# Performance work log

Measured on AMD Instinct MI355X. Metric: run time of the kernel, lower is better.

Reference implementation:

```python
import jax, jax.numpy as jnp
import numpy as np

H = W = 256  # hard-coded in the original nn.Fold(output_size=(256,256))


def _shift(x, dy, dx):
    """out[y, x] = x[y - dy, x - dx], zero outside. x: [B, H, W]."""
    xp = jnp.pad(x, ((0, 0), (1, 1), (1, 1)))
    return jax.lax.dynamic_slice(xp, (0, 1 - dy, 1 - dx), x.shape)


def setup_inputs() -> dict:
    key = jax.random.key(0)
    k1, k2, k3 = jax.random.split(key, 3)
    B = 64
    return {
        "affinity": jax.random.normal(k1, (B, 8, H, W), dtype=jnp.float32),
        "current_segmentation": jax.random.normal(k2, (B, 1, H, W), dtype=jnp.float32),
        "coarse_segmentation": jax.random.normal(k3, (B, 1, H, W), dtype=jnp.float32),
    }


def reference(affinity, current_segmentation, coarse_segmentation):
    # Normalize affinities by L1 sum over the 8 neighbor channels.
    abs_sum = jnp.sum(jnp.abs(affinity), axis=1, keepdims=True)
    raw_sum = jnp.sum(affinity, axis=1, keepdims=True)  # computed pre-normalization, as in source
    a = affinity / abs_sum
    # 9-tap spatially-varying kernel: 8 neighbors + synthesized center weight (1 - raw_sum).
    new_aff = jnp.concatenate([a[:, 0:4], 1.0 - raw_sum, a[:, 4:]], axis=1)  # [B,9,H,W]

    cur = current_segmentation[:, 0]  # [B,H,W]
    coa = coarse_segmentation[:, 0]   # [B,H,W]

    # unfold(seg)[k] at patch center q is seg[q + off_k]; fold scatters term_k[q] to q + off_k.
    out = jnp.zeros_like(cur)
    for k in range(9):
        dy, dx = k // 3 - 1, k % 3 - 1
        seg_k = coa if k == 4 else _shift(cur, -dy, -dx)   # gather neighbor (center from coarse)
        out = out + _shift(new_aff[:, k] * seg_k, dy, dx)  # overlap-add (fold)
    return out[:, None, :, :]  # [B,1,256,256]
```

## Files before the change

kernel.cpp:

```cpp
#include <hip/hip_runtime.h>

#define HH 256
#define WW 256
#define CC 8
#define TY 32
#define LW (WW + 2)
#define NSTRIP (HH / TY)

__global__ __launch_bounds__(256) void cspn_strip(
    const float* __restrict__ aff,
    const float* __restrict__ cur,
    const float* __restrict__ coa,
    float* __restrict__ out)
{
    __shared__ float ring[4][CC][LW];

    const int cpx = gridDim.x >> 3;
    int wg = blockIdx.x;
    wg = (wg & 7) * cpx + (wg >> 3);

    const int b  = wg >> 3;
    const int y0 = (wg & (NSTRIP - 1)) * TY;
    const int x  = threadIdx.x;

    if (threadIdx.x < 64) {
        const int s = threadIdx.x >> 4;
        const int c = (threadIdx.x >> 1) & 7;
        ring[s][c][(threadIdx.x & 1) ? (LW - 1) : 0] = 0.f;
    }

    const size_t plane = (size_t)HH * WW;
    const float* __restrict__ ab = aff + (size_t)b * CC * plane;
    const size_t img = (size_t)b * plane;

    float r[CC];
    {
        const int yy = y0 - 1;
        const bool inb = ((unsigned)yy < HH);
        #pragma unroll
        for (int c = 0; c < CC; ++c)
            r[c] = inb ? ab[c * plane + (size_t)yy * WW + x] : 0.f;
    }
    float rsum_prev = 0.f;

    __syncthreads();

    for (int y = y0 - 1; y <= y0 + TY; ++y) {
        float n[CC];
        const int yn = y + 1;
        const bool ldn = (yn <= y0 + TY) && ((unsigned)yn < HH);
        #pragma unroll
        for (int c = 0; c < CC; ++c)
            n[c] = ldn ? ab[c * plane + (size_t)yn * WW + x] : 0.f;

        const int j = y - 1;
        const bool emit = (j >= y0);
        float cj = 0.f, oj = 0.f;
        if (emit) {
            cj = cur[img + (size_t)j * WW + x];
            oj = coa[img + (size_t)j * WW + x];
        }

        float s = 0.f, rs = 0.f;
        #pragma unroll
        for (int c = 0; c < CC; ++c) { s += fabsf(r[c]); rs += r[c]; }
        const float invs = (s > 0.f) ? (1.0f / s) : 0.f;
        const int slot = (y + 4) & 3;
        #pragma unroll
        for (int c = 0; c < CC; ++c) ring[slot][c][x + 1] = r[c] * invs;

        __syncthreads();

        if (emit) {
            const int sp = (y + 4) & 3;
            const int sc = (y + 3) & 3;
            const int sm = (y + 2) & 3;
            const int xc = x + 1;
            const float sum =
                ring[sp][0][xc + 1] + ring[sp][1][xc] + ring[sp][2][xc - 1] +
                ring[sc][3][xc + 1]                   + ring[sc][4][xc - 1] +
                ring[sm][5][xc + 1] + ring[sm][6][xc] + ring[sm][7][xc - 1];
            out[img + (size_t)j * WW + x] = cj * sum + oj * (1.0f - rsum_prev);
        }

        rsum_prev = rs;
        #pragma unroll
        for (int c = 0; c < CC; ++c) r[c] = n[c];
    }
}

extern "C" void kernel_launch(void* const* d_in, const int* in_sizes, int n_in,
                              void* d_out, int out_size, void* d_ws, size_t ws_size,
                              hipStream_t stream) {
    const float* aff = (const float*)d_in[0];
    const float* cur = (const float*)d_in[1];
    const float* coa = (const float*)d_in[2];
    float* out = (float*)d_out;

    dim3 grid(64 * NSTRIP);
    dim3 block(256);
    cspn_strip<<<grid, block, 0, stream>>>(aff, cur, coa, out);
}
```

Measured before the change: 37.05 us.

## Process two rows per iteration with 512-thread blocks and six-slot ring

Each block now runs 512 threads, and the two 256-thread halves handle adjacent rows of the strip. This halves the serial loop trip count and the number of barriers per row. The ring buffer grows to six slots, and the raw per-pixel sum moves into shared memory so the previous row's sum can be read across thread groups. It costs more shared memory per block and adds modulo-6 slot arithmetic, and the larger blocks may lower the number of resident blocks.

```diff
diff --git a/kernel.cpp b/kernel.cpp
--- a/kernel.cpp
+++ b/kernel.cpp
@@ -7,13 +7,14 @@
 #define LW (WW + 2)
 #define NSTRIP (HH / TY)
 
-__global__ __launch_bounds__(256) void cspn_strip(
+__global__ __launch_bounds__(512, 4) void cspn_pair(
     const float* __restrict__ aff,
     const float* __restrict__ cur,
     const float* __restrict__ coa,
     float* __restrict__ out)
 {
-    __shared__ float ring[4][CC][LW];
+    __shared__ float ring[6][CC][LW];
+    __shared__ float rsring[6][WW];
 
     const int cpx = gridDim.x >> 3;
     int wg = blockIdx.x;
@@ -21,39 +22,41 @@
 
     const int b  = wg >> 3;
     const int y0 = (wg & (NSTRIP - 1)) * TY;
-    const int x  = threadIdx.x;
+    const int x  = threadIdx.x & 255;
+    const int g  = threadIdx.x >> 8;
 
-    if (threadIdx.x < 64) {
+    if (threadIdx.x < 96) {
         const int s = threadIdx.x >> 4;
-        const int c = (threadIdx.x >> 1) & 7;
-        ring[s][c][(threadIdx.x & 1) ? (LW - 1) : 0] = 0.f;
+        const int r = threadIdx.x & 15;
+        ring[s][r >> 1][(r & 1) ? (LW - 1) : 0] = 0.f;
     }
 
     const size_t plane = (size_t)HH * WW;
     const float* __restrict__ ab = aff + (size_t)b * CC * plane;
     const size_t img = (size_t)b * plane;
 
-    float r[CC];
+    float r_[CC];
     {
-        const int yy = y0 - 1;
+        const int yy = y0 - 1 + g;
         const bool inb = ((unsigned)yy < HH);
         #pragma unroll
         for (int c = 0; c < CC; ++c)
-            r[c] = inb ? ab[c * plane + (size_t)yy * WW + x] : 0.f;
+            r_[c] = inb ? ab[c * plane + (size_t)yy * WW + x] : 0.f;
     }
-    float rsum_prev = 0.f;
-
     __syncthreads();
 
-    for (int y = y0 - 1; y <= y0 + TY; ++y) {
-        float n[CC];
-        const int yn = y + 1;
+    for (int i = 0; i <= TY / 2; ++i) {
+        const int ya   = y0 - 1 + 2 * i;
+        const int yrow = ya + g;
+
+        float n_[CC];
+        const int yn = yrow + 2;
         const bool ldn = (yn <= y0 + TY) && ((unsigned)yn < HH);
         #pragma unroll
         for (int c = 0; c < CC; ++c)
-            n[c] = ldn ? ab[c * plane + (size_t)yn * WW + x] : 0.f;
+            n_[c] = ldn ? ab[c * plane + (size_t)yn * WW + x] : 0.f;
 
-        const int j = y - 1;
+        const int j = ya - 1 + g;
         const bool emit = (j >= y0);
         float cj = 0.f, oj = 0.f;
         if (emit) {
@@ -63,29 +66,30 @@
 
         float s = 0.f, rs = 0.f;
         #pragma unroll
-        for (int c = 0; c < CC; ++c) { s += fabsf(r[c]); rs += r[c]; }
+        for (int c = 0; c < CC; ++c) { s += fabsf(r_[c]); rs += r_[c]; }
         const float invs = (s > 0.f) ? (1.0f / s) : 0.f;
-        const int slot = (y + 4) & 3;
+        const int slot = (yrow + 12) % 6;
         #pragma unroll
-        for (int c = 0; c < CC; ++c) ring[slot][c][x + 1] = r[c] * invs;
+        for (int c = 0; c < CC; ++c) ring[slot][c][x + 1] = r_[c] * invs;
+        rsring[slot][x] = rs;
 
         __syncthreads();
 
         if (emit) {
-            const int sp = (y + 4) & 3;
-            const int sc = (y + 3) & 3;
-            const int sm = (y + 2) & 3;
+            const int sp = slot;
+            int sc = slot - 1; if (sc < 0) sc += 6;
+            int sm = slot - 2; if (sm < 0) sm += 6;
             const int xc = x + 1;
             const float sum =
                 ring[sp][0][xc + 1] + ring[sp][1][xc] + ring[sp][2][xc - 1] +
                 ring[sc][3][xc + 1]                   + ring[sc][4][xc - 1] +
                 ring[sm][5][xc + 1] + ring[sm][6][xc] + ring[sm][7][xc - 1];
-            out[img + (size_t)j * WW + x] = cj * sum + oj * (1.0f - rsum_prev);
+            const float rsj = rsring[sc][x];
+            out[img + (size_t)j * WW + x] = cj * sum + oj * (1.0f - rsj);
         }
 
-        rsum_prev = rs;
         #pragma unroll
-        for (int c = 0; c < CC; ++c) r[c] = n[c];
+        for (int c = 0; c < CC; ++c) r_[c] = n_[c];
     }
 }
 
@@ -98,6 +102,6 @@
     float* out = (float*)d_out;
 
     dim3 grid(64 * NSTRIP);
-    dim3 block(256);
-    cspn_strip<<<grid, block, 0, stream>>>(aff, cur, coa, out);
+    dim3 block(512);
+    cspn_pair<<<grid, block, 0, stream>>>(aff, cur, coa, out);
 }
```

Measured after the change: 33.73 us. 1.1x faster.
